# Performance work log

Hardware: AMD Instinct MI355X
Metric: run time of the kernel (lower is better)

Reference implementation:

```python
import jax, jax.numpy as jnp
import numpy as np
from jax import lax

EPS = 1e-6            # cfg.positive
GAUSS_DIM = (32, 32)  # cfg.iou_gauss_dim
TOP_K_CONF = 100      # cfg.nms_top_k_conf
TOP_K_IOU = 20        # cfg.nms_top_k_iou


def unnormal_gaussian(mask_shape, loc):
    # loc: [B, N, 4] = (cx, cy, w, h) in normalized [0,1] coords.
    # Unnormalized anisotropic gaussian rendered on an HxW grid.
    H, W = mask_shape
    cx, cy, w, h = loc[..., 0], loc[..., 1], loc[..., 2], loc[..., 3]
    ys = (jnp.arange(H, dtype=loc.dtype) + 0.5) / H
    xs = (jnp.arange(W, dtype=loc.dtype) + 0.5) / W
    dx = (xs[None, None, None, :] - cx[..., None, None]) / (w[..., None, None] + 1e-4)
    dy = (ys[None, None, :, None] - cy[..., None, None]) / (h[..., None, None] + 1e-4)
    return jnp.exp(-0.5 * (dx * dx + dy * dy))  # [B, N, H, W]


def _take2(t, idx):
    # twoIndexThree: t [B,N,D], idx [B,K] -> [B,K,D]
    return jnp.take_along_axis(t, idx[..., None], axis=1)


def detect(conf, loc, mask):
    # conf: [B,P] object scores; loc: [B,P,4]; mask: [B,P,Dm]
    sorted_conf, idx = lax.top_k(conf, TOP_K_CONF)
    sorted_loc = _take2(loc, idx)
    sorted_mask = _take2(mask, idx)
    g = unnormal_gaussian(GAUSS_DIM, sorted_loc)  # [B,N,Hg,Wg]
    # pairwise gaussian IoU: sum(min) / sum(max); use min+max == a+b identity
    inter = jnp.sum(jnp.minimum(g[:, :, None], g[:, None, :]), axis=(-2, -1))  # [B,N,N]
    s = jnp.sum(g, axis=(-2, -1))
    union = s[:, :, None] + s[:, None, :] - inter
    iou = inter / union
    iou_max = jnp.max(jnp.triu(iou, 1), axis=1)   # max overlap with any earlier (higher-conf) box
    _, keep = lax.top_k(-iou_max, TOP_K_IOU)      # keep K least-overlapping boxes
    return iou, sorted_loc, sorted_mask, sorted_conf, keep


def ae_scaled_loss(original, iou, keep, loc, conf):
    conf_matrix = conf[:, :, None] * conf[:, None, :]   # outer product [B,N,N]
    final_scale = iou * jnp.triu(conf_matrix, 1)
    kept_loc = _take2(loc, keep)                        # [B,K,4]
    # surrogate AutoEncoder per-box loss (AutoEncoder class not in source)
    ae_loss = jnp.mean(kept_loc ** 2, axis=-1)          # [B,K]
    B, N = final_scale.shape[0], final_scale.shape[1]
    K = keep.shape[1]
    ae_grid = jnp.zeros_like(final_scale).at[jnp.arange(B)[:, None], keep].set(
        jnp.broadcast_to(ae_loss[..., None], (B, K, N)))
    return jnp.mean(ae_grid * final_scale)


def variance_loss(original, loc, mask, conf, proto):
    B, C, H, W = original.shape
    Hp, Wp = proto.shape[1], proto.shape[2]
    ug = unnormal_gaussian((Hp, Wp), loc)                           # [B,K,Hp,Wp]
    assembled = jax.nn.sigmoid(jnp.einsum('bhwp,bkp->bkhw', proto, mask))  # lincomb
    attention = assembled * ug
    mc = attention * conf[:, :, None, None]                         # maskConfidence
    denom = jnp.sum(mc, axis=1, keepdims=True) + EPS
    final_conf = 1.0 - jnp.sum(mc * mc / denom, axis=1)             # [B,Hp,Wp]
    final_conf = jnp.where(jnp.isnan(final_conf), 0.0, final_conf)
    # bilinear, align_corners=False == jax linear resize (half-pixel centers)
    resized = jax.image.resize(final_conf[:, None], (B, 1, H, W), method='linear')[:, 0]
    total = jnp.sum(resized, axis=0)                                 # [H,W]
    wmean = jnp.einsum('bchw,bhw->chw', original, resized) / total
    sq = (original - wmean) ** 2
    wvar = sq * resized[:, None] / (total + EPS)
    return jnp.sum(wvar) / Hp * B


def reference(original, loc, conf, mask, proto):
    conf_p = jax.nn.softmax(conf, axis=2)[:, :, 1]
    iou, s_loc, s_mask, s_conf, keep = detect(conf_p, loc, mask)
    ae = ae_scaled_loss(original, iou, keep, s_loc, s_conf)
    k_loc = _take2(s_loc, keep)
    k_mask = _take2(s_mask, keep)
    k_conf = jnp.take_along_axis(s_conf, keep, axis=1)
    var = variance_loss(original, k_loc, k_mask, k_conf, proto)
    return jnp.stack([var, ae])  # [variance_loss, ae_loss]


def setup_inputs() -> dict:
    key = jax.random.key(0)
    k1, k2, k3, k4, k5, k6 = jax.random.split(key, 6)
    B, P, Dm = 2, 19248, 32
    H = W = 550
    Hp = Wp = 138
    original = jax.random.normal(k1, (B, 3, H, W), dtype=jnp.float32)
    centers = jax.random.uniform(k2, (B, P, 2), dtype=jnp.float32)
    sizes = jax.random.uniform(k3, (B, P, 2), dtype=jnp.float32, minval=0.1, maxval=0.5)
    loc = jnp.concatenate([centers, sizes], axis=-1)                 # (cx,cy,w,h)
    conf = jax.random.normal(k4, (B, P, 2), dtype=jnp.float32)
    mask = jax.random.normal(k5, (B, P, Dm), dtype=jnp.float32) * 0.2
    proto = jax.random.normal(k6, (B, Hp, Wp, Dm), dtype=jnp.float32) * 0.5
    return {"original": original, "loc": loc, "conf": conf, "mask": mask, "proto": proto}
```

## Files before the change

kernel.cpp:

```cpp
#include <hip/hip_runtime.h>
#include <hip/hip_bf16.h>
#include <math.h>

constexpr int B   = 2;
constexpr int P   = 19248;
constexpr int N   = 100;
constexpr int K   = 20;
constexpr int GD  = 32;
constexpr int GP  = GD * GD;
constexpr int HP  = 138;
constexpr int HPP = HP * HP;
constexpr int H   = 550;
constexpr int W   = 550;
constexpr int DM  = 32;
constexpr float EPS = 1e-6f;
constexpr int NBIN = 2048;
constexpr int CAND = 2048;
constexpr int NPAIR = N * (N - 1) / 2;

constexpr int OFS_IDX   = 0;
constexpr int OFS_SCONF = OFS_IDX   + B * N;
constexpr int OFS_SLOC  = OFS_SCONF + B * N;
constexpr int OFS_IOU   = OFS_SLOC  + B * N * 4;
constexpr int OFS_KLOC  = OFS_IOU   + B * N * N;
constexpr int OFS_KMASK = OFS_KLOC  + B * K * 4;
constexpr int OFS_KCONF = OFS_KMASK + B * K * DM;
constexpr int OFS_FC    = OFS_KCONF + B * K;

__global__ __launch_bounds__(1024) void k_topk(
    const float* __restrict__ conf, const float* __restrict__ loc,
    float* __restrict__ wsf, int* __restrict__ wsi, float* __restrict__ out) {
  const int b = blockIdx.x;
  const int t = threadIdx.x;
  constexpr int EPT = (P + 1023) / 1024;
  if (b == 0 && t < 2) out[t] = 0.0f;

  __shared__ int   hist[NBIN];
  __shared__ int   s_T, s_cnt;
  __shared__ float cv[CAND];
  __shared__ int   ci[CAND];
  __shared__ float outv[N];
  __shared__ int   outi[N];

  for (int q = t; q < NBIN; q += 1024) hist[q] = 0;
  if (t == 0) s_cnt = 0;
  __syncthreads();

  float v[EPT];
#pragma unroll
  for (int j = 0; j < EPT; j++) {
    int p = j * 1024 + t;
    if (p < P) {
      float c0 = conf[(b * P + p) * 2 + 0];
      float c1 = conf[(b * P + p) * 2 + 1];
      float m  = fmaxf(c0, c1);
      float e0 = expf(c0 - m), e1 = expf(c1 - m);
      v[j] = e1 / (e0 + e1);
      atomicAdd(&hist[__float_as_uint(v[j]) >> 19], 1);
    } else {
      v[j] = -1.0f;
    }
  }
  __syncthreads();

  if (t == 0) {
    int acc = 0, bin = NBIN - 1;
    for (; bin >= 0; bin--) { acc += hist[bin]; if (acc >= N) break; }
    s_T = bin;
  }
  __syncthreads();
  const int T = s_T;

#pragma unroll
  for (int j = 0; j < EPT; j++) {
    int p = j * 1024 + t;
    if (p < P && (int)(__float_as_uint(v[j]) >> 19) >= T) {
      int pos = atomicAdd(&s_cnt, 1);
      if (pos < CAND) { cv[pos] = v[j]; ci[pos] = p; }
    }
  }
  __syncthreads();
  const int M = min(s_cnt, CAND);

#pragma unroll
  for (int q = 0; q < CAND / 1024; q++) {
    int c = t + q * 1024;
    if (c < M) {
      float mv = cv[c]; int mi = ci[c];
      int rank = 0;
      for (int j = 0; j < M; j++) {
        float jv = cv[j]; int ji = ci[j];
        rank += (jv > mv || (jv == mv && ji < mi)) ? 1 : 0;
      }
      if (rank < N) { outv[rank] = mv; outi[rank] = mi; }
    }
  }
  __syncthreads();

  if (t < N) {
    wsi[OFS_IDX + b * N + t]   = outi[t];
    wsf[OFS_SCONF + b * N + t] = outv[t];
  }
  if (t < N * 4) {
    int k = t >> 2, d = t & 3;
    wsf[OFS_SLOC + (b * N + k) * 4 + d] = loc[(b * P + outi[k]) * 4 + d];
  }
}

__global__ __launch_bounds__(256) void k_iou(float* __restrict__ wsf) {
  const int blk = blockIdx.x;
  const int b = blk / NPAIR;
  const int r = blk - b * NPAIR;
  int i = (int)((199.0f - sqrtf((float)(39601 - 8 * r))) * 0.5f);
  i = min(max(i, 0), N - 2);
  while (i < N - 2 && ((i + 1) * (2 * N - 2 - i)) / 2 <= r) i++;
  while (i > 0 && (i * (2 * N - 1 - i)) / 2 > r) i--;
  const int j = i + 1 + (r - (i * (2 * N - 1 - i)) / 2);

  const int t = threadIdx.x;
  const float* li = &wsf[OFS_SLOC + (b * N + i) * 4];
  const float* lj = &wsf[OFS_SLOC + (b * N + j) * 4];
  const float cxi = li[0], cyi = li[1], wi = li[2], hi = li[3];
  const float cxj = lj[0], cyj = lj[1], wj = lj[2], hj = lj[3];

  float smin = 0.0f, ssi = 0.0f, ssj = 0.0f;
#pragma unroll
  for (int q = 0; q < 4; q++) {
    int pix = t + q * 256;
    int y = pix >> 5, x = pix & 31;
    float xs = (x + 0.5f) / 32.0f, ys = (y + 0.5f) / 32.0f;
    float dxi = (xs - cxi) / (wi + 1e-4f);
    float dyi = (ys - cyi) / (hi + 1e-4f);
    float gi = expf(-0.5f * (dxi * dxi + dyi * dyi));
    float dxj = (xs - cxj) / (wj + 1e-4f);
    float dyj = (ys - cyj) / (hj + 1e-4f);
    float gj = expf(-0.5f * (dxj * dxj + dyj * dyj));
    smin += fminf(gi, gj);
    ssi += gi;
    ssj += gj;
  }
  for (int off = 32; off > 0; off >>= 1) {
    smin += __shfl_down(smin, off);
    ssi  += __shfl_down(ssi, off);
    ssj  += __shfl_down(ssj, off);
  }
  __shared__ float sp[3][4];
  if ((t & 63) == 0) {
    int w4 = t >> 6;
    sp[0][w4] = smin; sp[1][w4] = ssi; sp[2][w4] = ssj;
  }
  __syncthreads();
  if (t == 0) {
    float inter = sp[0][0] + sp[0][1] + sp[0][2] + sp[0][3];
    float si    = sp[1][0] + sp[1][1] + sp[1][2] + sp[1][3];
    float sj    = sp[2][0] + sp[2][1] + sp[2][2] + sp[2][3];
    wsf[OFS_IOU + (b * N + i) * N + j] = inter / (si + sj - inter);
  }
}

__global__ __launch_bounds__(1024) void k_select(
    const float* __restrict__ mask, float* __restrict__ wsf,
    int* __restrict__ wsi, float* __restrict__ out) {
  const int b = blockIdx.x;
  const int t = threadIdx.x;
  __shared__ float siou[N * N];
  __shared__ float sconf[N];
  __shared__ unsigned int mbits[N];
  __shared__ int   keep[K];
  __shared__ float coef[K];
  __shared__ float red[16];

  for (int idx = t; idx < N * N; idx += 1024) {
    int row = idx / N, col = idx - row * N;
    siou[idx] = (col > row) ? wsf[OFS_IOU + b * N * N + idx] : 0.0f;
  }
  if (t < N) { sconf[t] = wsf[OFS_SCONF + b * N + t]; mbits[t] = 0u; }
  __syncthreads();

  for (int idx = t; idx < N * N; idx += 1024) {
    int col = idx % N;
    atomicMax(&mbits[col], __float_as_uint(siou[idx]));
  }
  __syncthreads();

  if (t < N) {
    unsigned int vb = mbits[t];
    int rank = 0;
    for (int j = 0; j < N; j++) {
      unsigned int jb = mbits[j];
      rank += (jb < vb || (jb == vb && j < t)) ? 1 : 0;
    }
    if (rank < K) keep[rank] = t;
  }
  __syncthreads();

  if (t < K) {
    int r = keep[t];
    float c = sconf[r];
    wsf[OFS_KCONF + b * K + t] = c;
    const float* kl = &wsf[OFS_SLOC + (b * N + r) * 4];
    float ael = 0.25f * (kl[0] * kl[0] + kl[1] * kl[1] + kl[2] * kl[2] + kl[3] * kl[3]);
    coef[t] = ael * c;
  }
  if (t < K * 4) {
    int k = t >> 2, d = t & 3;
    wsf[OFS_KLOC + (b * K + k) * 4 + d] = wsf[OFS_SLOC + (b * N + keep[k]) * 4 + d];
  }
  if (t < K * DM) {
    int k = t >> 5, d = t & 31;
    int orig = wsi[OFS_IDX + b * N + keep[k]];
    wsf[OFS_KMASK + (b * K + k) * DM + d] = mask[(b * P + orig) * DM + d];
  }
  __syncthreads();

  float acc = 0.0f;
  for (int kc = t; kc < K * N; kc += 1024) {
    int k = kc / N, c = kc - k * N;
    int r = keep[k];
    if (c > r) acc += siou[r * N + c] * sconf[c] * coef[k];
  }
  for (int off = 32; off > 0; off >>= 1) acc += __shfl_down(acc, off);
  if ((t & 63) == 0) red[t >> 6] = acc;
  __syncthreads();
  if (t == 0) {
    float s = 0.0f;
    for (int w2 = 0; w2 < 16; w2++) s += red[w2];
    atomicAdd(out + 1, s * (1.0f / (float)(B * N * N)));
  }
}

__global__ __launch_bounds__(256) void k_fc(
    const float* __restrict__ proto, float* __restrict__ wsf) {
  const int b = blockIdx.y;
  const int t = threadIdx.x;
  const int pix = blockIdx.x * 256 + t;
  __shared__ float kl[K * 4];
  __shared__ float kc[K];
  __shared__ float km[K * DM];
  for (int q = t; q < K * 4; q += 256) kl[q] = wsf[OFS_KLOC + b * K * 4 + q];
  for (int q = t; q < K; q += 256) kc[q] = wsf[OFS_KCONF + b * K + q];
  for (int q = t; q < K * DM; q += 256) km[q] = wsf[OFS_KMASK + b * K * DM + q];
  __syncthreads();
  if (pix >= HPP) return;
  const int h = pix / HP, w2 = pix - h * HP;

  float pv[DM];
  const float4* pp = (const float4*)&proto[(size_t)(b * HPP + pix) * DM];
#pragma unroll
  for (int q = 0; q < DM / 4; q++) {
    float4 f = pp[q];
    pv[q * 4 + 0] = f.x; pv[q * 4 + 1] = f.y;
    pv[q * 4 + 2] = f.z; pv[q * 4 + 3] = f.w;
  }
  const float ysv = (h + 0.5f) / 138.0f;
  const float xsv = (w2 + 0.5f) / 138.0f;
  float sum1 = 0.0f, sum2 = 0.0f;
#pragma unroll
  for (int k = 0; k < K; k++) {
    float dot = 0.0f;
#pragma unroll
    for (int d = 0; d < DM; d++) dot += pv[d] * km[k * DM + d];
    float a  = 1.0f / (1.0f + expf(-dot));
    float dx = (xsv - kl[k * 4 + 0]) / (kl[k * 4 + 2] + 1e-4f);
    float dy = (ysv - kl[k * 4 + 1]) / (kl[k * 4 + 3] + 1e-4f);
    float ug = expf(-0.5f * (dx * dx + dy * dy));
    float att = a * ug * kc[k];
    sum1 += att;
    sum2 += att * att;
  }
  float fc = 1.0f - sum2 / (sum1 + EPS);
  if (fc != fc) fc = 0.0f;
  wsf[OFS_FC + b * HPP + pix] = fc;
}

__global__ __launch_bounds__(256) void k_var(
    const float* __restrict__ orig, const float* __restrict__ wsf,
    float* __restrict__ out) {
  const int t = threadIdx.x;
  float acc = 0.0f;
  for (int pix = blockIdx.x * 256 + t; pix < H * W; pix += 256 * 256) {
    const int h = pix / W, w2 = pix - h * W;
    const float sc = 138.0f / 550.0f;
    float sy = (h + 0.5f) * sc - 0.5f;
    float sx = (w2 + 0.5f) * sc - 0.5f;
    float fy0 = floorf(sy), fx0 = floorf(sx);
    float wy = sy - fy0, wx = sx - fx0;
    int y0 = max(0, (int)fy0), y1 = min(HP - 1, (int)fy0 + 1);
    int x0 = max(0, (int)fx0), x1 = min(HP - 1, (int)fx0 + 1);
    float r0, r1;
    {
      const float* fc = &wsf[OFS_FC + 0 * HPP];
      float v00 = fc[y0 * HP + x0], v01 = fc[y0 * HP + x1];
      float v10 = fc[y1 * HP + x0], v11 = fc[y1 * HP + x1];
      float top = v00 + (v01 - v00) * wx;
      float bot = v10 + (v11 - v10) * wx;
      r0 = top + (bot - top) * wy;
    }
    {
      const float* fc = &wsf[OFS_FC + 1 * HPP];
      float v00 = fc[y0 * HP + x0], v01 = fc[y0 * HP + x1];
      float v10 = fc[y1 * HP + x0], v11 = fc[y1 * HP + x1];
      float top = v00 + (v01 - v00) * wx;
      float bot = v10 + (v11 - v10) * wx;
      r1 = top + (bot - top) * wy;
    }
    float total = r0 + r1;
    float inv_t = 1.0f / total;
    float inv_te = 1.0f / (total + EPS);
#pragma unroll
    for (int c = 0; c < 3; c++) {
      float o0 = orig[((0 * 3 + c) * H + h) * W + w2];
      float o1 = orig[((1 * 3 + c) * H + h) * W + w2];
      float wm = (o0 * r0 + o1 * r1) * inv_t;
      float d0 = o0 - wm, d1 = o1 - wm;
      acc += (d0 * d0 * r0 + d1 * d1 * r1) * inv_te;
    }
  }
  for (int off = 32; off > 0; off >>= 1) acc += __shfl_down(acc, off);
  __shared__ float sp[4];
  if ((t & 63) == 0) sp[t >> 6] = acc;
  __syncthreads();
  if (t == 0)
    atomicAdd(out + 0, (sp[0] + sp[1] + sp[2] + sp[3]) * ((float)B / (float)HP));
}

extern "C" void kernel_launch(void* const* d_in, const int* in_sizes, int n_in,
                              void* d_out, int out_size, void* d_ws,
                              size_t ws_size, hipStream_t stream) {
  (void)in_sizes; (void)n_in; (void)out_size; (void)ws_size;
  const float* original = (const float*)d_in[0];
  const float* loc      = (const float*)d_in[1];
  const float* conf     = (const float*)d_in[2];
  const float* mask     = (const float*)d_in[3];
  const float* proto    = (const float*)d_in[4];
  float* out = (float*)d_out;
  float* wsf = (float*)d_ws;
  int*   wsi = (int*)d_ws;

  k_topk<<<B, 1024, 0, stream>>>(conf, loc, wsf, wsi, out);
  k_iou<<<B * NPAIR, 256, 0, stream>>>(wsf);
  k_select<<<B, 1024, 0, stream>>>(mask, wsf, wsi, out);
  k_fc<<<dim3((HPP + 255) / 256, B), 256, 0, stream>>>(proto, wsf);
  k_var<<<256, 256, 0, stream>>>(original, wsf, out);
}
```

Measured before the change: 132.1 us.

## Fuse all stages into one persistent kernel with software grid barriers

Replaces five separate kernel launches with a single persistent kernel of 256 blocks that moves between stages through an atomic-counter grid barrier. The top-k histogram and candidate gathering now spread across the whole grid using global atomics instead of one block per batch. The pairwise IoU work maps one wavefront per pair rather than one block per pair, and two memsets reset the barrier counter and the histogram. This removes launch overhead and the serial single-block top-k, but adds grid-barrier spin costs, idle blocks during the per-batch stages, and a risk of deadlock if not all 256 blocks are resident at once.

```diff
diff --git a/kernel.cpp b/kernel.cpp
--- a/kernel.cpp
+++ b/kernel.cpp
@@ -1,13 +1,10 @@
 #include <hip/hip_runtime.h>
-#include <hip/hip_bf16.h>
 #include <math.h>
 
 constexpr int B   = 2;
 constexpr int P   = 19248;
 constexpr int N   = 100;
 constexpr int K   = 20;
-constexpr int GD  = 32;
-constexpr int GP  = GD * GD;
 constexpr int HP  = 138;
 constexpr int HPP = HP * HP;
 constexpr int H   = 550;
@@ -18,310 +15,349 @@
 constexpr int CAND = 2048;
 constexpr int NPAIR = N * (N - 1) / 2;
 
-constexpr int OFS_IDX   = 0;
-constexpr int OFS_SCONF = OFS_IDX   + B * N;
+constexpr int GRID = 256;
+constexpr int TPB  = 512;
+constexpr int GT   = GRID * TPB;
+
+constexpr int IOFS_IDX  = 0;
+constexpr int OFS_SCONF = IOFS_IDX + B * N;
 constexpr int OFS_SLOC  = OFS_SCONF + B * N;
-constexpr int OFS_IOU   = OFS_SLOC  + B * N * 4;
-constexpr int OFS_KLOC  = OFS_IOU   + B * N * N;
-constexpr int OFS_KMASK = OFS_KLOC  + B * K * 4;
+constexpr int OFS_IOU   = OFS_SLOC + B * N * 4;
+constexpr int OFS_KLOC  = OFS_IOU + B * N * N;
+constexpr int OFS_KMASK = OFS_KLOC + B * K * 4;
 constexpr int OFS_KCONF = OFS_KMASK + B * K * DM;
 constexpr int OFS_FC    = OFS_KCONF + B * K;
 
-__global__ __launch_bounds__(1024) void k_topk(
-    const float* __restrict__ conf, const float* __restrict__ loc,
-    float* __restrict__ wsf, int* __restrict__ wsi, float* __restrict__ out) {
-  const int b = blockIdx.x;
-  const int t = threadIdx.x;
-  constexpr int EPT = (P + 1023) / 1024;
-  if (b == 0 && t < 2) out[t] = 0.0f;
-
-  __shared__ int   hist[NBIN];
-  __shared__ int   s_T, s_cnt;
-  __shared__ float cv[CAND];
-  __shared__ int   ci[CAND];
-  __shared__ float outv[N];
-  __shared__ int   outi[N];
-
-  for (int q = t; q < NBIN; q += 1024) hist[q] = 0;
-  if (t == 0) s_cnt = 0;
+constexpr int OFS_BAR = OFS_IOU;
+
+constexpr int SC_HIST  = OFS_FC;
+constexpr int SC_CNT   = SC_HIST + B * NBIN;
+constexpr int SC_CANDI = SC_CNT + B;
+constexpr int SC_CANDV = SC_CANDI + B * CAND;
+
+struct SmemB { int h[NBIN]; int c[NBIN / 16]; int T[B]; };
+struct SmemC { float cv[CAND]; int ci[CAND]; float outv[N]; int outi[N]; };
+struct SmemE { float siou[N * N]; float sconf[N]; unsigned int mbits[N];
+               int keep[K]; float coef[K]; float red[TPB / 64]; };
+struct SmemF { float kl[B * K * 4]; float kc[B * K]; float km[B * K * DM]; };
+union  SmemU { SmemB b; SmemC c; SmemE e; SmemF f; float red[TPB / 64]; };
+
+__device__ __forceinline__ void gridbar(unsigned int* bar) {
   __syncthreads();
-
-  float v[EPT];
-#pragma unroll
-  for (int j = 0; j < EPT; j++) {
-    int p = j * 1024 + t;
-    if (p < P) {
-      float c0 = conf[(b * P + p) * 2 + 0];
-      float c1 = conf[(b * P + p) * 2 + 1];
-      float m  = fmaxf(c0, c1);
-      float e0 = expf(c0 - m), e1 = expf(c1 - m);
-      v[j] = e1 / (e0 + e1);
-      atomicAdd(&hist[__float_as_uint(v[j]) >> 19], 1);
-    } else {
-      v[j] = -1.0f;
-    }
+  if (threadIdx.x == 0) {
+    __threadfence();
+    unsigned int tk = __hip_atomic_fetch_add(bar, 1u, __ATOMIC_RELEASE,
+                                             __HIP_MEMORY_SCOPE_AGENT);
+    unsigned int target = (tk / (unsigned)GRID + 1u) * (unsigned)GRID;
+    while (__hip_atomic_load(bar, __ATOMIC_ACQUIRE,
+                             __HIP_MEMORY_SCOPE_AGENT) < target)
+      __builtin_amdgcn_s_sleep(2);
+    __threadfence();
   }
   __syncthreads();
-
-  if (t == 0) {
-    int acc = 0, bin = NBIN - 1;
-    for (; bin >= 0; bin--) { acc += hist[bin]; if (acc >= N) break; }
-    s_T = bin;
-  }
-  __syncthreads();
-  const int T = s_T;
-
-#pragma unroll
-  for (int j = 0; j < EPT; j++) {
-    int p = j * 1024 + t;
-    if (p < P && (int)(__float_as_uint(v[j]) >> 19) >= T) {
-      int pos = atomicAdd(&s_cnt, 1);
-      if (pos < CAND) { cv[pos] = v[j]; ci[pos] = p; }
-    }
-  }
-  __syncthreads();
-  const int M = min(s_cnt, CAND);
-
-#pragma unroll
-  for (int q = 0; q < CAND / 1024; q++) {
-    int c = t + q * 1024;
-    if (c < M) {
-      float mv = cv[c]; int mi = ci[c];
+}
+
+__global__ __launch_bounds__(TPB, 2) void k_fused(
+    const float* __restrict__ original, const float* __restrict__ loc,
+    const float* __restrict__ conf, const float* __restrict__ mask,
+    const float* __restrict__ proto, float* wsf, int* wsi, float* out) {
+  const int t   = threadIdx.x;
+  const int bid = blockIdx.x;
+  const int g   = bid * TPB + t;
+  unsigned int* bar = (unsigned int*)&wsi[OFS_BAR];
+  __shared__ SmemU sm;
+
+  if (g == 0) { out[0] = 0.0f; out[1] = 0.0f; }
+  {
+    const float2* c2 = (const float2*)conf;
+    for (int q = g; q < B * P; q += GT) {
+      float2 c = c2[q];
+      float m  = fmaxf(c.x, c.y);
+      float e0 = expf(c.x - m), e1 = expf(c.y - m);
+      float v  = e1 / (e0 + e1);
+      int b = (q >= P) ? 1 : 0;
+      atomicAdd(&wsi[SC_HIST + b * NBIN + (int)(__float_as_uint(v) >> 19)], 1);
+    }
+  }
+  gridbar(bar);
+
+  for (int b = 0; b < B; b++) {
+    for (int q = t; q < NBIN; q += TPB) sm.b.h[q] = wsi[SC_HIST + b * NBIN + q];
+    __syncthreads();
+    if (t < NBIN / 16) {
+      int s = 0;
+      for (int u = 0; u < 16; u++) s += sm.b.h[t * 16 + u];
+      sm.b.c[t] = s;
+    }
+    __syncthreads();
+    if (t == 0) {
+      int acc = 0, ch = NBIN / 16 - 1;
+      for (; ch >= 0; ch--) { int cs = sm.b.c[ch]; if (acc + cs >= N) break; acc += cs; }
+      int T = -1;
+      if (ch >= 0) {
+        int bin = ch * 16 + 15;
+        for (; bin >= ch * 16; bin--) { acc += sm.b.h[bin]; if (acc >= N) break; }
+        T = bin;
+      }
+      sm.b.T[b] = T;
+    }
+    __syncthreads();
+  }
+  {
+    const int T0 = sm.b.T[0], T1 = sm.b.T[1];
+    const float2* c2 = (const float2*)conf;
+    for (int q = g; q < B * P; q += GT) {
+      float2 c = c2[q];
+      float m  = fmaxf(c.x, c.y);
+      float e0 = expf(c.x - m), e1 = expf(c.y - m);
+      float v  = e1 / (e0 + e1);
+      int b = (q >= P) ? 1 : 0;
+      if ((int)(__float_as_uint(v) >> 19) >= (b ? T1 : T0)) {
+        int pos = atomicAdd(&wsi[SC_CNT + b], 1);
+        if (pos < CAND) {
+          wsf[SC_CANDV + b * CAND + pos] = v;
+          wsi[SC_CANDI + b * CAND + pos] = q - b * P;
+        }
+      }
+    }
+  }
+  gridbar(bar);
+
+  if (bid < B) {
+    const int b = bid;
+    const int M = min(wsi[SC_CNT + b], CAND);
+    for (int q = t; q < M; q += TPB) {
+      sm.c.cv[q] = wsf[SC_CANDV + b * CAND + q];
+      sm.c.ci[q] = wsi[SC_CANDI + b * CAND + q];
+    }
+    __syncthreads();
+    for (int c = t; c < M; c += TPB) {
+      float mv = sm.c.cv[c]; int mi = sm.c.ci[c];
       int rank = 0;
-      for (int j = 0; j < M; j++) {
-        float jv = cv[j]; int ji = ci[j];
+      for (int j2 = 0; j2 < M; j2++) {
+        float jv = sm.c.cv[j2]; int ji = sm.c.ci[j2];
         rank += (jv > mv || (jv == mv && ji < mi)) ? 1 : 0;
       }
-      if (rank < N) { outv[rank] = mv; outi[rank] = mi; }
-    }
-  }
-  __syncthreads();
-
-  if (t < N) {
-    wsi[OFS_IDX + b * N + t]   = outi[t];
-    wsf[OFS_SCONF + b * N + t] = outv[t];
-  }
-  if (t < N * 4) {
-    int k = t >> 2, d = t & 3;
-    wsf[OFS_SLOC + (b * N + k) * 4 + d] = loc[(b * P + outi[k]) * 4 + d];
-  }
-}
-
-__global__ __launch_bounds__(256) void k_iou(float* __restrict__ wsf) {
-  const int blk = blockIdx.x;
-  const int b = blk / NPAIR;
-  const int r = blk - b * NPAIR;
-  int i = (int)((199.0f - sqrtf((float)(39601 - 8 * r))) * 0.5f);
-  i = min(max(i, 0), N - 2);
-  while (i < N - 2 && ((i + 1) * (2 * N - 2 - i)) / 2 <= r) i++;
-  while (i > 0 && (i * (2 * N - 1 - i)) / 2 > r) i--;
-  const int j = i + 1 + (r - (i * (2 * N - 1 - i)) / 2);
-
-  const int t = threadIdx.x;
-  const float* li = &wsf[OFS_SLOC + (b * N + i) * 4];
-  const float* lj = &wsf[OFS_SLOC + (b * N + j) * 4];
-  const float cxi = li[0], cyi = li[1], wi = li[2], hi = li[3];
-  const float cxj = lj[0], cyj = lj[1], wj = lj[2], hj = lj[3];
-
-  float smin = 0.0f, ssi = 0.0f, ssj = 0.0f;
-#pragma unroll
-  for (int q = 0; q < 4; q++) {
-    int pix = t + q * 256;
-    int y = pix >> 5, x = pix & 31;
-    float xs = (x + 0.5f) / 32.0f, ys = (y + 0.5f) / 32.0f;
-    float dxi = (xs - cxi) / (wi + 1e-4f);
-    float dyi = (ys - cyi) / (hi + 1e-4f);
-    float gi = expf(-0.5f * (dxi * dxi + dyi * dyi));
-    float dxj = (xs - cxj) / (wj + 1e-4f);
-    float dyj = (ys - cyj) / (hj + 1e-4f);
-    float gj = expf(-0.5f * (dxj * dxj + dyj * dyj));
-    smin += fminf(gi, gj);
-    ssi += gi;
-    ssj += gj;
-  }
-  for (int off = 32; off > 0; off >>= 1) {
-    smin += __shfl_down(smin, off);
-    ssi  += __shfl_down(ssi, off);
-    ssj  += __shfl_down(ssj, off);
-  }
-  __shared__ float sp[3][4];
-  if ((t & 63) == 0) {
-    int w4 = t >> 6;
-    sp[0][w4] = smin; sp[1][w4] = ssi; sp[2][w4] = ssj;
-  }
-  __syncthreads();
-  if (t == 0) {
-    float inter = sp[0][0] + sp[0][1] + sp[0][2] + sp[0][3];
-    float si    = sp[1][0] + sp[1][1] + sp[1][2] + sp[1][3];
-    float sj    = sp[2][0] + sp[2][1] + sp[2][2] + sp[2][3];
-    wsf[OFS_IOU + (b * N + i) * N + j] = inter / (si + sj - inter);
-  }
-}
-
-__global__ __launch_bounds__(1024) void k_select(
-    const float* __restrict__ mask, float* __restrict__ wsf,
-    int* __restrict__ wsi, float* __restrict__ out) {
-  const int b = blockIdx.x;
-  const int t = threadIdx.x;
-  __shared__ float siou[N * N];
-  __shared__ float sconf[N];
-  __shared__ unsigned int mbits[N];
-  __shared__ int   keep[K];
-  __shared__ float coef[K];
-  __shared__ float red[16];
-
-  for (int idx = t; idx < N * N; idx += 1024) {
-    int row = idx / N, col = idx - row * N;
-    siou[idx] = (col > row) ? wsf[OFS_IOU + b * N * N + idx] : 0.0f;
-  }
-  if (t < N) { sconf[t] = wsf[OFS_SCONF + b * N + t]; mbits[t] = 0u; }
-  __syncthreads();
-
-  for (int idx = t; idx < N * N; idx += 1024) {
-    int col = idx % N;
-    atomicMax(&mbits[col], __float_as_uint(siou[idx]));
-  }
-  __syncthreads();
-
-  if (t < N) {
-    unsigned int vb = mbits[t];
-    int rank = 0;
-    for (int j = 0; j < N; j++) {
-      unsigned int jb = mbits[j];
-      rank += (jb < vb || (jb == vb && j < t)) ? 1 : 0;
-    }
-    if (rank < K) keep[rank] = t;
-  }
-  __syncthreads();
-
-  if (t < K) {
-    int r = keep[t];
-    float c = sconf[r];
-    wsf[OFS_KCONF + b * K + t] = c;
-    const float* kl = &wsf[OFS_SLOC + (b * N + r) * 4];
-    float ael = 0.25f * (kl[0] * kl[0] + kl[1] * kl[1] + kl[2] * kl[2] + kl[3] * kl[3]);
-    coef[t] = ael * c;
-  }
-  if (t < K * 4) {
-    int k = t >> 2, d = t & 3;
-    wsf[OFS_KLOC + (b * K + k) * 4 + d] = wsf[OFS_SLOC + (b * N + keep[k]) * 4 + d];
-  }
-  if (t < K * DM) {
-    int k = t >> 5, d = t & 31;
-    int orig = wsi[OFS_IDX + b * N + keep[k]];
-    wsf[OFS_KMASK + (b * K + k) * DM + d] = mask[(b * P + orig) * DM + d];
-  }
-  __syncthreads();
-
-  float acc = 0.0f;
-  for (int kc = t; kc < K * N; kc += 1024) {
-    int k = kc / N, c = kc - k * N;
-    int r = keep[k];
-    if (c > r) acc += siou[r * N + c] * sconf[c] * coef[k];
-  }
-  for (int off = 32; off > 0; off >>= 1) acc += __shfl_down(acc, off);
-  if ((t & 63) == 0) red[t >> 6] = acc;
-  __syncthreads();
-  if (t == 0) {
-    float s = 0.0f;
-    for (int w2 = 0; w2 < 16; w2++) s += red[w2];
-    atomicAdd(out + 1, s * (1.0f / (float)(B * N * N)));
-  }
-}
-
-__global__ __launch_bounds__(256) void k_fc(
-    const float* __restrict__ proto, float* __restrict__ wsf) {
-  const int b = blockIdx.y;
-  const int t = threadIdx.x;
-  const int pix = blockIdx.x * 256 + t;
-  __shared__ float kl[K * 4];
-  __shared__ float kc[K];
-  __shared__ float km[K * DM];
-  for (int q = t; q < K * 4; q += 256) kl[q] = wsf[OFS_KLOC + b * K * 4 + q];
-  for (int q = t; q < K; q += 256) kc[q] = wsf[OFS_KCONF + b * K + q];
-  for (int q = t; q < K * DM; q += 256) km[q] = wsf[OFS_KMASK + b * K * DM + q];
-  __syncthreads();
-  if (pix >= HPP) return;
-  const int h = pix / HP, w2 = pix - h * HP;
-
-  float pv[DM];
-  const float4* pp = (const float4*)&proto[(size_t)(b * HPP + pix) * DM];
-#pragma unroll
-  for (int q = 0; q < DM / 4; q++) {
-    float4 f = pp[q];
-    pv[q * 4 + 0] = f.x; pv[q * 4 + 1] = f.y;
-    pv[q * 4 + 2] = f.z; pv[q * 4 + 3] = f.w;
-  }
-  const float ysv = (h + 0.5f) / 138.0f;
-  const float xsv = (w2 + 0.5f) / 138.0f;
-  float sum1 = 0.0f, sum2 = 0.0f;
-#pragma unroll
-  for (int k = 0; k < K; k++) {
-    float dot = 0.0f;
-#pragma unroll
-    for (int d = 0; d < DM; d++) dot += pv[d] * km[k * DM + d];
-    float a  = 1.0f / (1.0f + expf(-dot));
-    float dx = (xsv - kl[k * 4 + 0]) / (kl[k * 4 + 2] + 1e-4f);
-    float dy = (ysv - kl[k * 4 + 1]) / (kl[k * 4 + 3] + 1e-4f);
-    float ug = expf(-0.5f * (dx * dx + dy * dy));
-    float att = a * ug * kc[k];
-    sum1 += att;
-    sum2 += att * att;
-  }
-  float fc = 1.0f - sum2 / (sum1 + EPS);
-  if (fc != fc) fc = 0.0f;
-  wsf[OFS_FC + b * HPP + pix] = fc;
-}
-
-__global__ __launch_bounds__(256) void k_var(
-    const float* __restrict__ orig, const float* __restrict__ wsf,
-    float* __restrict__ out) {
-  const int t = threadIdx.x;
-  float acc = 0.0f;
-  for (int pix = blockIdx.x * 256 + t; pix < H * W; pix += 256 * 256) {
-    const int h = pix / W, w2 = pix - h * W;
-    const float sc = 138.0f / 550.0f;
-    float sy = (h + 0.5f) * sc - 0.5f;
-    float sx = (w2 + 0.5f) * sc - 0.5f;
-    float fy0 = floorf(sy), fx0 = floorf(sx);
-    float wy = sy - fy0, wx = sx - fx0;
-    int y0 = max(0, (int)fy0), y1 = min(HP - 1, (int)fy0 + 1);
-    int x0 = max(0, (int)fx0), x1 = min(HP - 1, (int)fx0 + 1);
-    float r0, r1;
-    {
-      const float* fc = &wsf[OFS_FC + 0 * HPP];
-      float v00 = fc[y0 * HP + x0], v01 = fc[y0 * HP + x1];
-      float v10 = fc[y1 * HP + x0], v11 = fc[y1 * HP + x1];
-      float top = v00 + (v01 - v00) * wx;
-      float bot = v10 + (v11 - v10) * wx;
-      r0 = top + (bot - top) * wy;
-    }
-    {
-      const float* fc = &wsf[OFS_FC + 1 * HPP];
-      float v00 = fc[y0 * HP + x0], v01 = fc[y0 * HP + x1];
-      float v10 = fc[y1 * HP + x0], v11 = fc[y1 * HP + x1];
-      float top = v00 + (v01 - v00) * wx;
-      float bot = v10 + (v11 - v10) * wx;
-      r1 = top + (bot - top) * wy;
-    }
-    float total = r0 + r1;
-    float inv_t = 1.0f / total;
-    float inv_te = 1.0f / (total + EPS);
-#pragma unroll
-    for (int c = 0; c < 3; c++) {
-      float o0 = orig[((0 * 3 + c) * H + h) * W + w2];
-      float o1 = orig[((1 * 3 + c) * H + h) * W + w2];
-      float wm = (o0 * r0 + o1 * r1) * inv_t;
-      float d0 = o0 - wm, d1 = o1 - wm;
-      acc += (d0 * d0 * r0 + d1 * d1 * r1) * inv_te;
-    }
-  }
-  for (int off = 32; off > 0; off >>= 1) acc += __shfl_down(acc, off);
-  __shared__ float sp[4];
-  if ((t & 63) == 0) sp[t >> 6] = acc;
-  __syncthreads();
-  if (t == 0)
-    atomicAdd(out + 0, (sp[0] + sp[1] + sp[2] + sp[3]) * ((float)B / (float)HP));
+      if (rank < N) { sm.c.outv[rank] = mv; sm.c.outi[rank] = mi; }
+    }
+    __syncthreads();
+    if (t < N) {
+      wsi[IOFS_IDX + b * N + t]  = sm.c.outi[t];
+      wsf[OFS_SCONF + b * N + t] = sm.c.outv[t];
+    }
+    if (t < N * 4) {
+      int k = t >> 2, d = t & 3;
+      wsf[OFS_SLOC + (b * N + k) * 4 + d] = loc[(b * P + sm.c.outi[k]) * 4 + d];
+    }
+  }
+  gridbar(bar);
+
+  {
+    const int wid  = (bid << 3) + (t >> 6);
+    const int lane = t & 63;
+    for (int pr = wid; pr < B * NPAIR; pr += GRID * 8) {
+      const int b = (pr >= NPAIR) ? 1 : 0;
+      const int r = pr - b * NPAIR;
+      int i = (int)((199.0f - sqrtf((float)(39601 - 8 * r))) * 0.5f);
+      i = min(max(i, 0), N - 2);
+      while (i < N - 2 && ((i + 1) * (2 * N - 2 - i)) / 2 <= r) i++;
+      while (i > 0 && (i * (2 * N - 1 - i)) / 2 > r) i--;
+      const int j = i + 1 + (r - (i * (2 * N - 1 - i)) / 2);
+
+      const float4 li = *(const float4*)&wsf[OFS_SLOC + (b * N + i) * 4];
+      const float4 lj = *(const float4*)&wsf[OFS_SLOC + (b * N + j) * 4];
+
+      float smn[4], ssi[4], ssj[4];
+#pragma unroll
+      for (int w4 = 0; w4 < 4; w4++) {
+        smn[w4] = 0.0f; ssi[w4] = 0.0f; ssj[w4] = 0.0f;
+#pragma unroll
+        for (int q = 0; q < 4; q++) {
+          int pix = lane + (w4 << 6) + (q << 8);
+          int y = pix >> 5, x = pix & 31;
+          float xs = (x + 0.5f) / 32.0f, ys = (y + 0.5f) / 32.0f;
+          float dxi = (xs - li.x) / (li.z + 1e-4f);
+          float dyi = (ys - li.y) / (li.w + 1e-4f);
+          float gi = expf(-0.5f * (dxi * dxi + dyi * dyi));
+          float dxj = (xs - lj.x) / (lj.z + 1e-4f);
+          float dyj = (ys - lj.y) / (lj.w + 1e-4f);
+          float gj = expf(-0.5f * (dxj * dxj + dyj * dyj));
+          smn[w4] += fminf(gi, gj);
+          ssi[w4] += gi;
+          ssj[w4] += gj;
+        }
+      }
+#pragma unroll
+      for (int off = 32; off > 0; off >>= 1) {
+#pragma unroll
+        for (int w4 = 0; w4 < 4; w4++) {
+          smn[w4] += __shfl_down(smn[w4], off);
+          ssi[w4] += __shfl_down(ssi[w4], off);
+          ssj[w4] += __shfl_down(ssj[w4], off);
+        }
+      }
+      if (lane == 0) {
+        float inter = smn[0] + smn[1] + smn[2] + smn[3];
+        float si    = ssi[0] + ssi[1] + ssi[2] + ssi[3];
+        float sj    = ssj[0] + ssj[1] + ssj[2] + ssj[3];
+        wsf[OFS_IOU + (b * N + i) * N + j] = inter / (si + sj - inter);
+      }
+    }
+  }
+  gridbar(bar);
+
+  if (bid < B) {
+    const int b = bid;
+    for (int idx = t; idx < N * N; idx += TPB) {
+      int row = idx / N, col = idx - row * N;
+      float vv = 0.0f;
+      if (col > row) vv = wsf[OFS_IOU + b * N * N + idx];
+      sm.e.siou[idx] = vv;
+    }
+    if (t < N) { sm.e.sconf[t] = wsf[OFS_SCONF + b * N + t]; sm.e.mbits[t] = 0u; }
+    __syncthreads();
+    for (int idx = t; idx < N * N; idx += TPB) {
+      int col = idx % N;
+      atomicMax(&sm.e.mbits[col], __float_as_uint(sm.e.siou[idx]));
+    }
+    __syncthreads();
+    if (t < N) {
+      unsigned int vb = sm.e.mbits[t];
+      int rank = 0;
+      for (int j2 = 0; j2 < N; j2++) {
+        unsigned int jb = sm.e.mbits[j2];
+        rank += (jb < vb || (jb == vb && j2 < t)) ? 1 : 0;
+      }
+      if (rank < K) sm.e.keep[rank] = t;
+    }
+    __syncthreads();
+    if (t < K) {
+      int r = sm.e.keep[t];
+      float c = sm.e.sconf[r];
+      wsf[OFS_KCONF + b * K + t] = c;
+      const float* kl2 = &wsf[OFS_SLOC + (b * N + r) * 4];
+      float ael = 0.25f * (kl2[0] * kl2[0] + kl2[1] * kl2[1] +
+                           kl2[2] * kl2[2] + kl2[3] * kl2[3]);
+      sm.e.coef[t] = ael * c;
+    }
+    if (t < K * 4) {
+      int k = t >> 2, d = t & 3;
+      wsf[OFS_KLOC + (b * K + k) * 4 + d] =
+          wsf[OFS_SLOC + (b * N + sm.e.keep[k]) * 4 + d];
+    }
+    for (int q = t; q < K * DM; q += TPB) {
+      int k = q >> 5, d = q & 31;
+      int orig_i = wsi[IOFS_IDX + b * N + sm.e.keep[k]];
+      wsf[OFS_KMASK + (b * K + k) * DM + d] = mask[(b * P + orig_i) * DM + d];
+    }
+    __syncthreads();
+
+    float acc = 0.0f;
+    for (int kc = t; kc < K * N; kc += TPB) {
+      int k = kc / N, c = kc - k * N;
+      int r = sm.e.keep[k];
+      if (c > r) acc += sm.e.siou[r * N + c] * sm.e.sconf[c] * sm.e.coef[k];
+    }
+    for (int off = 32; off > 0; off >>= 1) acc += __shfl_down(acc, off);
+    if ((t & 63) == 0) sm.e.red[t >> 6] = acc;
+    __syncthreads();
+    if (t == 0) {
+      float s = 0.0f;
+      for (int w2 = 0; w2 < TPB / 64; w2++) s += sm.e.red[w2];
+      atomicAdd(out + 1, s * (1.0f / (float)(B * N * N)));
+    }
+  }
+  gridbar(bar);
+
+  {
+    for (int q = t; q < B * K * 4; q += TPB)  sm.f.kl[q] = wsf[OFS_KLOC + q];
+    for (int q = t; q < B * K; q += TPB)      sm.f.kc[q] = wsf[OFS_KCONF + q];
+    for (int q = t; q < B * K * DM; q += TPB) sm.f.km[q] = wsf[OFS_KMASK + q];
+    __syncthreads();
+    for (int px = g; px < B * HPP; px += GT) {
+      const int b = (px >= HPP) ? 1 : 0;
+      const int pix = px - b * HPP;
+      const int h = pix / HP, w2 = pix - h * HP;
+      float pv[DM];
+      const float4* pp = (const float4*)&proto[(size_t)px * DM];
+#pragma unroll
+      for (int q = 0; q < DM / 4; q++) {
+        float4 f4 = pp[q];
+        pv[q * 4 + 0] = f4.x; pv[q * 4 + 1] = f4.y;
+        pv[q * 4 + 2] = f4.z; pv[q * 4 + 3] = f4.w;
+      }
+      const float ysv = (h + 0.5f) / 138.0f;
+      const float xsv = (w2 + 0.5f) / 138.0f;
+      float sum1 = 0.0f, sum2 = 0.0f;
+#pragma unroll
+      for (int k = 0; k < K; k++) {
+        float dot = 0.0f;
+#pragma unroll
+        for (int d = 0; d < DM; d++) dot += pv[d] * sm.f.km[(b * K + k) * DM + d];
+        float a  = 1.0f / (1.0f + expf(-dot));
+        float dx = (xsv - sm.f.kl[(b * K + k) * 4 + 0]) / (sm.f.kl[(b * K + k) * 4 + 2] + 1e-4f);
+        float dy = (ysv - sm.f.kl[(b * K + k) * 4 + 1]) / (sm.f.kl[(b * K + k) * 4 + 3] + 1e-4f);
+        float ug = expf(-0.5f * (dx * dx + dy * dy));
+        float att = a * ug * sm.f.kc[b * K + k];
+        sum1 += att;
+        sum2 += att * att;
+      }
+      float fc = 1.0f - sum2 / (sum1 + EPS);
+      if (fc != fc) fc = 0.0f;
+      wsf[OFS_FC + px] = fc;
+    }
+  }
+  gridbar(bar);
+
+  {
+    float acc = 0.0f;
+    for (int pix = g; pix < H * W; pix += GT) {
+      const int h = pix / W, w2 = pix - h * W;
+      const float scl = 138.0f / 550.0f;
+      float sy = (h + 0.5f) * scl - 0.5f;
+      float sx = (w2 + 0.5f) * scl - 0.5f;
+      float fy0 = floorf(sy), fx0 = floorf(sx);
+      float wy = sy - fy0, wx = sx - fx0;
+      int y0 = max(0, (int)fy0), y1 = min(HP - 1, (int)fy0 + 1);
+      int x0 = max(0, (int)fx0), x1 = min(HP - 1, (int)fx0 + 1);
+      float r0, r1;
+      {
+        const float* fc = &wsf[OFS_FC + 0 * HPP];
+        float v00 = fc[y0 * HP + x0], v01 = fc[y0 * HP + x1];
+        float v10 = fc[y1 * HP + x0], v11 = fc[y1 * HP + x1];
+        float top = v00 + (v01 - v00) * wx;
+        float bot = v10 + (v11 - v10) * wx;
+        r0 = top + (bot - top) * wy;
+      }
+      {
+        const float* fc = &wsf[OFS_FC + 1 * HPP];
+        float v00 = fc[y0 * HP + x0], v01 = fc[y0 * HP + x1];
+        float v10 = fc[y1 * HP + x0], v11 = fc[y1 * HP + x1];
+        float top = v00 + (v01 - v00) * wx;
+        float bot = v10 + (v11 - v10) * wx;
+        r1 = top + (bot - top) * wy;
+      }
+      float total = r0 + r1;
+      float inv_t  = 1.0f / total;
+      float inv_te = 1.0f / (total + EPS);
+#pragma unroll
+      for (int c = 0; c < 3; c++) {
+        float o0 = original[((0 * 3 + c) * H + h) * W + w2];
+        float o1 = original[((1 * 3 + c) * H + h) * W + w2];
+        float wm = (o0 * r0 + o1 * r1) * inv_t;
+        float d0 = o0 - wm, d1 = o1 - wm;
+        acc += (d0 * d0 * r0 + d1 * d1 * r1) * inv_te;
+      }
+    }
+    for (int off = 32; off > 0; off >>= 1) acc += __shfl_down(acc, off);
+    if ((t & 63) == 0) sm.red[t >> 6] = acc;
+    __syncthreads();
+    if (t == 0) {
+      float s = 0.0f;
+      for (int w3 = 0; w3 < TPB / 64; w3++) s += sm.red[w3];
+      atomicAdd(out + 0, s * ((float)B / (float)HP));
+    }
+  }
 }
 
 extern "C" void kernel_launch(void* const* d_in, const int* in_sizes, int n_in,
@@ -337,9 +373,10 @@
   float* wsf = (float*)d_ws;
   int*   wsi = (int*)d_ws;
 
-  k_topk<<<B, 1024, 0, stream>>>(conf, loc, wsf, wsi, out);
-  k_iou<<<B * NPAIR, 256, 0, stream>>>(wsf);
-  k_select<<<B, 1024, 0, stream>>>(mask, wsf, wsi, out);
-  k_fc<<<dim3((HPP + 255) / 256, B), 256, 0, stream>>>(proto, wsf);
-  k_var<<<256, 256, 0, stream>>>(original, wsf, out);
+  hipMemsetAsync((char*)d_ws + (size_t)OFS_BAR * 4, 0, 4, stream);
+  hipMemsetAsync((char*)d_ws + (size_t)SC_HIST * 4, 0,
+                 (size_t)(B * NBIN + B) * 4, stream);
+
+  k_fused<<<GRID, TPB, 0, stream>>>(original, loc, conf, mask, proto,
+                                    wsf, wsi, out);
 }
```

Measured after the change: 333.4 us. +152.3%, slower.
